# Kernel optimization log

Measured on AMD Instinct MI355X. Metric: run time of the kernel, lower is better.

Reference implementation:

```python
import jax, jax.numpy as jnp
import numpy as np

N_TOKENS = 4096   # flat tokens (batch*seq)
TOP_K = 2         # experts per token
N_EXPERTS = 8
D_IN = 1024
D_OUT = 1024


def setup_inputs() -> dict:
    key = jax.random.key(0)
    k1, k2, k3, k4 = jax.random.split(key, 4)
    x = jax.random.normal(k1, (N_TOKENS, D_IN), jnp.float32)
    # ParallelExperts.weight is [E, out, in] with std=0.02; forward permutes to [E, in, out].
    expert_weights = jax.random.normal(k2, (N_EXPERTS, D_IN, D_OUT), jnp.float32) * 0.02
    # Random top-k expert assignment per (token, slot); flat index = token*k + slot.
    expert_ids = jax.random.randint(k3, (N_TOKENS * TOP_K,), 0, N_EXPERTS)
    order = jnp.argsort(expert_ids, stable=True)           # dispatch order, sorted by expert
    sorted_expert_idxs = expert_ids[order].astype(jnp.int32)
    sorted_scattered_idxs = order.astype(jnp.int32)        # flat (token*k+slot) index of each sorted row
    counts = jnp.bincount(expert_ids, length=N_EXPERTS)
    expert_offsets = jnp.cumsum(counts).astype(jnp.int32)  # kernel bookkeeping (unused in math)
    padded_block_idxs = jnp.zeros((1,), jnp.int32)         # kernel bookkeeping (unused in math)
    gates = jax.nn.softmax(jax.random.normal(k4, (N_TOKENS, TOP_K), jnp.float32), axis=-1)
    return {
        "x": x,
        "expert_weights": expert_weights,
        "gates": gates,
        "k": TOP_K,
        "sorted_expert_idxs": sorted_expert_idxs,
        "sorted_scattered_idxs": sorted_scattered_idxs,
        "padded_block_idxs": padded_block_idxs,
        "expert_offsets": expert_offsets,
    }


def _scatter2scatter(x, W, sorted_expert_idxs, sorted_scattered_idxs, k):
    """out_flat[j] = x[j // k] @ W[expert_of_flat_slot_j]; rows processed in sorted order."""
    n_experts = W.shape[0]
    tok = sorted_scattered_idxs // k          # source token for each sorted row (x not grouped)
    xg = x[tok]                               # [N*k, d_in] gathered in expert-sorted order
    out_g = jnp.zeros((xg.shape[0], W.shape[-1]), x.dtype)
    for e in range(n_experts):                # small fixed expert loop (masked grouped GEMM)
        mask = (sorted_expert_idxs == e).astype(x.dtype)[:, None]
        out_g = out_g + (xg * mask) @ W[e]
    # scatter back to flat (token*k+slot) order (y not grouped)
    return jnp.zeros_like(out_g).at[sorted_scattered_idxs].set(out_g)


def reference(x, expert_weights, gates, k, sorted_expert_idxs, sorted_scattered_idxs,
              padded_block_idxs, expert_offsets):
    out_flat = _scatter2scatter(x, expert_weights, sorted_expert_idxs, sorted_scattered_idxs, k)
    # gate-weighted combine: bmm(gates[:,None,:], out.view(N,k,d)).squeeze(1)
    n, kk = gates.shape
    out_expanded = out_flat.reshape(n, kk, -1)
    return jnp.einsum("nk,nkd->nd", gates, out_expanded)
```

## Files before the change

### kernel.cpp

```cpp
#include <hip/hip_runtime.h>
#include <hip/hip_bf16.h>
#include <stdint.h>

#define N_TOK   4096
#define TOPK    2
#define NSORT   (N_TOK * TOPK)
#define NEXP    8
#define DIM     1024

#define BM 128
#define BN 64
#define BK 64

typedef __attribute__((ext_vector_type(8))) short bfrag;
typedef __attribute__((ext_vector_type(4))) float f32x4;

static __device__ __forceinline__ unsigned short f2bf(float f) {
  __hip_bfloat16 h = __float2bfloat16(f);
  return __builtin_bit_cast(unsigned short, h);
}
static __device__ __forceinline__ float bf2f(unsigned short u) {
  unsigned int v = ((unsigned int)u) << 16;
  return __builtin_bit_cast(float, v);
}

static __device__ __forceinline__ void gload16(void* lds_base, const void* gsrc) {
  __builtin_amdgcn_global_load_lds(
      (const __attribute__((address_space(1))) void*)gsrc,
      (__attribute__((address_space(3))) void*)lds_base, 16, 0, 0);
}

__global__ __launch_bounds__(256) void k_gather_x(
    const float* __restrict__ x, const int* __restrict__ ssi, const int* __restrict__ kp,
    unsigned short* __restrict__ xg, float* __restrict__ zbuf)
{
  const int row = blockIdx.x;
  const int t = threadIdx.x;
  const int kk = kp[0];
  const int tok = ssi[row] / kk;
  float4 v = ((const float4*)(x + (size_t)tok * DIM))[t];
  ushort4 o;
  o.x = f2bf(v.x); o.y = f2bf(v.y); o.z = f2bf(v.z); o.w = f2bf(v.w);
  ((ushort4*)(xg + (size_t)row * DIM))[t] = o;
  if (row == 0) { zbuf[t] = 0.0f; zbuf[256 + t] = 0.0f; }
}

__global__ __launch_bounds__(256) void k_transp_w(
    const float* __restrict__ W, unsigned short* __restrict__ WT)
{
  __shared__ float tile[64][65];
  const int nb = blockIdx.x;
  const int kb = blockIdx.y;
  const int e  = blockIdx.z;
  const int t = threadIdx.x;
  const float* src = W + (((size_t)e * DIM) + (size_t)kb * 64) * DIM + nb * 64;
  #pragma unroll
  for (int p = 0; p < 4; ++p) {
    int q = p * 256 + t;
    int i = q >> 4;
    int j4 = q & 15;
    float4 v = *(const float4*)(src + (size_t)i * DIM + j4 * 4);
    tile[i][j4 * 4 + 0] = v.x; tile[i][j4 * 4 + 1] = v.y;
    tile[i][j4 * 4 + 2] = v.z; tile[i][j4 * 4 + 3] = v.w;
  }
  __syncthreads();
  unsigned short* dst = WT + (((size_t)e * DIM) + (size_t)nb * 64) * DIM + kb * 64;
  #pragma unroll
  for (int p = 0; p < 4; ++p) {
    int q = p * 256 + t;
    int j = q >> 4;
    int i4 = q & 15;
    ushort4 o;
    o.x = f2bf(tile[i4 * 4 + 0][j]);
    o.y = f2bf(tile[i4 * 4 + 1][j]);
    o.z = f2bf(tile[i4 * 4 + 2][j]);
    o.w = f2bf(tile[i4 * 4 + 3][j]);
    *(ushort4*)(dst + (size_t)j * DIM + i4 * 4) = o;
  }
}

__global__ __launch_bounds__(256, 4) void k_moe_gemm(
    const unsigned short* __restrict__ xg,
    const unsigned short* __restrict__ WT,
    const int* __restrict__ sei, const int* __restrict__ ssi,
    const float* __restrict__ zbuf,
    unsigned short* __restrict__ outw)
{
  __shared__ unsigned short lA[BM * BK];
  __shared__ unsigned short lB[BN * BK];
  __shared__ int s_sei[BM];
  __shared__ int s_ssi[BM];

  const int swz = (blockIdx.x & 7) * 128 + (blockIdx.x >> 3);
  const int rt = swz >> 4;
  const int ct = swz & 15;
  const int t = threadIdx.x;
  const int lane = t & 63;
  const int w = t >> 6;
  const int wr = w >> 1;
  const int wc = w & 1;

  if (t < BM) {
    s_sei[t] = sei[rt * BM + t];
    s_ssi[t] = ssi[rt * BM + t];
  }
  __syncthreads();

  const int e0 = s_sei[0];
  const int e1 = s_sei[BM - 1];
  const int nsteps = (e1 - e0 + 1) * (DIM / BK);

  f32x4 acc[4][2];
  #pragma unroll
  for (int m = 0; m < 4; ++m)
    #pragma unroll
    for (int n = 0; n < 2; ++n)
      acc[m][n] = (f32x4){0.f, 0.f, 0.f, 0.f};

  const int g = lane >> 4;
  const int r = lane & 15;

  int rA[4], kA[4], rB[2], kB[2];
  #pragma unroll
  for (int i = 0; i < 4; ++i) {
    int o = (4 * w + i) * 1024 + lane * 16;
    int osw = o ^ (((o >> 7) & 7) << 4);
    rA[i] = osw >> 7; kA[i] = osw & 127;
  }
  #pragma unroll
  for (int i = 0; i < 2; ++i) {
    int o = (2 * w + i) * 1024 + lane * 16;
    int osw = o ^ (((o >> 7) & 7) << 4);
    rB[i] = osw >> 7; kB[i] = osw & 127;
  }

  const char *ap[4], *bp[2];
  int ecur = 0x7fffffff;
  auto setup = [&](int e) {
    #pragma unroll
    for (int i = 0; i < 4; ++i)
      ap[i] = (s_sei[rA[i]] == e)
          ? (const char*)(xg + ((size_t)(rt * BM + rA[i])) * DIM) + kA[i] : (const char*)zbuf;
    #pragma unroll
    for (int i = 0; i < 2; ++i)
      bp[i] = (const char*)(WT + (((size_t)e * DIM) + ct * BN + rB[i]) * DIM) + kB[i];
  };
  auto stage = [&](int s) {
    const int e = e0 + (s >> 4);
    if (e != ecur) { ecur = e; setup(e); }
    const int koff = (s & 15) * 128;
    #pragma unroll
    for (int i = 0; i < 4; ++i)
      gload16((char*)lA + (4 * w + i) * 1024, ap[i] + koff);
    #pragma unroll
    for (int i = 0; i < 2; ++i)
      gload16((char*)lB + (2 * w + i) * 1024, bp[i] + koff);
  };

  for (int s = 0; s < nsteps; ++s) {
    stage(s);
    __syncthreads();
    #pragma unroll
    for (int kh = 0; kh < 2; ++kh) {
      const int kbyte = (kh * 32 + 8 * g) * 2;
      bfrag af[4], bfv[2];
      #pragma unroll
      for (int m = 0; m < 4; ++m) {
        const int row = wr * 64 + m * 16 + r;
        int o = (row << 7) + kbyte;
        o ^= ((row & 7) << 4);
        af[m] = *(const bfrag*)((const char*)lA + o);
      }
      #pragma unroll
      for (int n = 0; n < 2; ++n) {
        const int nn = wc * 32 + n * 16 + r;
        int o = (nn << 7) + kbyte;
        o ^= ((nn & 7) << 4);
        bfv[n] = *(const bfrag*)((const char*)lB + o);
      }
      #pragma unroll
      for (int m = 0; m < 4; ++m)
        #pragma unroll
        for (int n = 0; n < 2; ++n)
          acc[m][n] = __builtin_amdgcn_mfma_f32_16x16x32_bf16(af[m], bfv[n], acc[m][n], 0, 0, 0);
    }
    __syncthreads();
  }

  #pragma unroll
  for (int m = 0; m < 4; ++m) {
    #pragma unroll
    for (int q = 0; q < 4; ++q) {
      const int rl = wr * 64 + m * 16 + g * 4 + q;
      const int orow = s_ssi[rl];
      unsigned short* od = outw + (size_t)orow * DIM + ct * BN + wc * 32 + r;
      #pragma unroll
      for (int n = 0; n < 2; ++n)
        od[n * 16] = f2bf(acc[m][n][q]);
    }
  }
}

__global__ __launch_bounds__(256) void k_combine(
    const unsigned short* __restrict__ outw, const float* __restrict__ gates,
    const int* __restrict__ kp, float* __restrict__ out)
{
  const int tk = blockIdx.x;
  const int t = threadIdx.x;
  const int kk = kp[0];
  float4 o = {0.f, 0.f, 0.f, 0.f};
  for (int s = 0; s < kk; ++s) {
    const float gte = gates[tk * kk + s];
    ushort4 a = ((const ushort4*)(outw + ((size_t)tk * kk + s) * DIM))[t];
    o.x += gte * bf2f(a.x);
    o.y += gte * bf2f(a.y);
    o.z += gte * bf2f(a.z);
    o.w += gte * bf2f(a.w);
  }
  ((float4*)(out + (size_t)tk * DIM))[t] = o;
}

extern "C" void kernel_launch(void* const* d_in, const int* in_sizes, int n_in,
                              void* d_out, int out_size, void* d_ws, size_t ws_size,
                              hipStream_t stream)
{
  const float* x     = (const float*)d_in[0];
  const float* W     = (const float*)d_in[1];
  const float* gates = (const float*)d_in[2];
  const int* kp      = (const int*)d_in[3];
  const int* sei     = (const int*)d_in[4];
  const int* ssi     = (const int*)d_in[5];

  const size_t MB = 1024 * 1024;
  if (ws_size < 48 * MB + 4096) return;

  char* ws = (char*)d_ws;
  unsigned short* xg   = (unsigned short*)(ws);
  unsigned short* WT   = (unsigned short*)(ws + 16 * MB);
  unsigned short* outw = (unsigned short*)(ws + 32 * MB);
  float* zbuf          = (float*)(ws + 48 * MB);

  k_gather_x<<<NSORT, 256, 0, stream>>>(x, ssi, kp, xg, zbuf);
  k_transp_w<<<dim3(16, 16, 8), 256, 0, stream>>>(W, WT);
  k_moe_gemm<<<(NSORT / BM) * (DIM / BN), 256, 0, stream>>>(xg, WT, sei, ssi, zbuf, outw);
  k_combine<<<N_TOK, 256, 0, stream>>>(outw, gates, kp, (float*)d_out);
}
```

Before: 61.30 us.

## Triple-buffer LDS tiles in MoE GEMM with async global-to-LDS prefetch

Replaces the single LDS buffer (load, sync, compute, sync) with a 3-stage ring buffer. Three k-steps are prefetched ahead via global_load_lds, and the loop waits on vmcnt(12) so that only the oldest stage must have landed before compute. The aim is to hide global memory latency behind the MFMA work. LDS per block grows to about 72KB and the occupancy hint drops from 4 to 2 blocks per SIMD. Steps past the end are clamped to re-issue the last stage, which costs redundant loads.

```diff
diff --git a/kernel.cpp b/kernel.cpp
--- a/kernel.cpp
+++ b/kernel.cpp
@@ -79,15 +79,14 @@
   }
 }
 
-__global__ __launch_bounds__(256, 4) void k_moe_gemm(
+__global__ __launch_bounds__(256, 2) void k_moe_gemm(
     const unsigned short* __restrict__ xg,
     const unsigned short* __restrict__ WT,
     const int* __restrict__ sei, const int* __restrict__ ssi,
     const float* __restrict__ zbuf,
     unsigned short* __restrict__ outw)
 {
-  __shared__ unsigned short lA[BM * BK];
-  __shared__ unsigned short lB[BN * BK];
+  __shared__ char lds[3][(BM + BN) * BK * 2];
   __shared__ int s_sei[BM];
   __shared__ int s_ssi[BM];
 
@@ -145,21 +144,29 @@
     for (int i = 0; i < 2; ++i)
       bp[i] = (const char*)(WT + (((size_t)e * DIM) + ct * BN + rB[i]) * DIM) + kB[i];
   };
-  auto stage = [&](int s) {
+  auto stage = [&](int s, int b) {
     const int e = e0 + (s >> 4);
     if (e != ecur) { ecur = e; setup(e); }
     const int koff = (s & 15) * 128;
+    char* base = (char*)lds[b];
     #pragma unroll
     for (int i = 0; i < 4; ++i)
-      gload16((char*)lA + (4 * w + i) * 1024, ap[i] + koff);
+      gload16(base + (4 * w + i) * 1024, ap[i] + koff);
     #pragma unroll
     for (int i = 0; i < 2; ++i)
-      gload16((char*)lB + (2 * w + i) * 1024, bp[i] + koff);
+      gload16(base + 16384 + (2 * w + i) * 1024, bp[i] + koff);
   };
 
+  stage(0, 0); stage(1, 1); stage(2, 2);
+
+  int cur = 0;
   for (int s = 0; s < nsteps; ++s) {
-    stage(s);
-    __syncthreads();
+    asm volatile("s_waitcnt vmcnt(12)" ::: "memory");
+    __builtin_amdgcn_s_barrier();
+    __builtin_amdgcn_sched_barrier(0);
+
+    const char* pA = (const char*)lds[cur];
+    const char* pB = (const char*)lds[cur] + 16384;
     #pragma unroll
     for (int kh = 0; kh < 2; ++kh) {
       const int kbyte = (kh * 32 + 8 * g) * 2;
@@ -169,14 +176,14 @@
         const int row = wr * 64 + m * 16 + r;
         int o = (row << 7) + kbyte;
         o ^= ((row & 7) << 4);
-        af[m] = *(const bfrag*)((const char*)lA + o);
+        af[m] = *(const bfrag*)(pA + o);
       }
       #pragma unroll
       for (int n = 0; n < 2; ++n) {
         const int nn = wc * 32 + n * 16 + r;
         int o = (nn << 7) + kbyte;
         o ^= ((nn & 7) << 4);
-        bfv[n] = *(const bfrag*)((const char*)lB + o);
+        bfv[n] = *(const bfrag*)(pB + o);
       }
       #pragma unroll
       for (int m = 0; m < 4; ++m)
@@ -184,7 +191,15 @@
         for (int n = 0; n < 2; ++n)
           acc[m][n] = __builtin_amdgcn_mfma_f32_16x16x32_bf16(af[m], bfv[n], acc[m][n], 0, 0, 0);
     }
-    __syncthreads();
+
+    asm volatile("s_waitcnt lgkmcnt(0)" ::: "memory");
+    __builtin_amdgcn_s_barrier();
+    __builtin_amdgcn_sched_barrier(0);
+
+    int sn = s + 3;
+    if (sn > nsteps - 1) sn = nsteps - 1;
+    stage(sn, cur);
+    cur = (cur == 2) ? 0 : cur + 1;
   }
 
   #pragma unroll
```

New measurement: 78.32 us. 1.28x slower.
